# Kernel tuning notes

Hardware: AMD Instinct MI355X
Metric: run time of the kernel (lower is better)

The kernel has to match this reference:

```python
import jax, jax.numpy as jnp
import numpy as np

N_NODES = 100000
N_EDGES = 3200000


def gcn_conv(x, src, dst, ew, W, b, num_nodes):
    """PyG GCNConv: h = x@W; out[dst] += norm * h[src]; norm = d^-1/2[src]*w*d^-1/2[dst].
    src/dst/ew must already include self-loops (weight 1)."""
    h = x @ W  # [N, F_out]
    deg = jax.ops.segment_sum(ew, dst, num_segments=num_nodes)  # weighted in-degree
    dinv = jnp.where(deg > 0, jax.lax.rsqrt(deg), 0.0)
    norm = dinv[src] * ew * dinv[dst]  # [E]
    msg = h[src] * norm[:, None]  # [E, F_out] gather + scale
    out = jax.ops.segment_sum(msg, dst, num_segments=num_nodes)  # scatter-add
    return out + b


def setup_inputs() -> dict:
    key = jax.random.key(0)
    k1, k2, k3, k4, k5 = jax.random.split(key, 5)
    x = jax.random.normal(k1, (N_NODES, 35), dtype=jnp.float32)
    edge_index = jax.random.randint(k2, (2, N_EDGES), 0, N_NODES, dtype=jnp.int64)
    edge_weight = jax.random.uniform(k3, (N_EDGES,), dtype=jnp.float32)
    W1 = jax.random.normal(k4, (35, 64), dtype=jnp.float32) * (1.0 / np.sqrt(35))
    b1 = jnp.zeros((64,), dtype=jnp.float32)
    W2 = jax.random.normal(k5, (64, 2), dtype=jnp.float32) * (1.0 / np.sqrt(64))
    b2 = jnp.zeros((2,), dtype=jnp.float32)
    return {"x": x, "edge_index": edge_index, "edge_weight": edge_weight,
            "W1": W1, "b1": b1, "W2": W2, "b2": b2}


def reference(x, edge_index, edge_weight, W1, b1, W2, b2):
    n = x.shape[0]
    # add self-loops with weight 1 (PyG default fill_value=1), static shapes
    loop = jnp.arange(n, dtype=edge_index.dtype)
    src = jnp.concatenate([edge_index[0], loop])
    dst = jnp.concatenate([edge_index[1], loop])
    ew = jnp.concatenate([edge_weight, jnp.ones((n,), dtype=edge_weight.dtype)])

    h = jax.nn.relu(gcn_conv(x, src, dst, ew, W1, b1, n))
    h = gcn_conv(h, src, dst, ew, W2, b2, n)
    return jax.nn.log_softmax(h, axis=1)
```

## Files before the change

### kernel.cpp

```cpp
#include <hip/hip_runtime.h>
#include <hip/hip_fp16.h>
#include <math.h>

#define FIN 35
#define F1  64
#define BSZ 256
#define BSH 8
#define GSH 7
#define MAXNB 512
#define PCH 8192
#define SCAP 12288

__global__ void k_hist(const int* __restrict__ dst, int* __restrict__ cmat,
                       int E, int NB, int NCHUNK) {
    __shared__ int h[MAXNB];
    int c = blockIdx.x, t = threadIdx.x;
    for (int i = t; i < NB; i += 256) h[i] = 0;
    __syncthreads();
    int e0 = c * PCH, e1 = min(e0 + PCH, E);
    bool al = ((size_t)(dst + e0) & 15) == 0;
    int nv = al ? ((e1 - e0) >> 2) : 0;
    const int4* d4 = (const int4*)(dst + e0);
    for (int i = t; i < nv; i += 256) {
        int4 v = d4[i];
        atomicAdd(&h[v.x >> BSH], 1); atomicAdd(&h[v.y >> BSH], 1);
        atomicAdd(&h[v.z >> BSH], 1); atomicAdd(&h[v.w >> BSH], 1);
    }
    for (int e = e0 + (nv << 2) + t; e < e1; e += 256) atomicAdd(&h[dst[e] >> BSH], 1);
    __syncthreads();
    for (int i = t; i < NB; i += 256) cmat[(size_t)i * NCHUNK + c] = h[i];
}

__global__ void k_scan_row(int* __restrict__ cmat, int* __restrict__ rsum, int NCHUNK) {
    __shared__ int s[512];
    int b = blockIdx.x, t = threadIdx.x;
    int v = (t < NCHUNK) ? cmat[(size_t)b * NCHUNK + t] : 0;
    s[t] = v;
    __syncthreads();
    #pragma unroll
    for (int off = 1; off < 512; off <<= 1) {
        int tv = (t >= off) ? s[t - off] : 0;
        __syncthreads();
        s[t] += tv;
        __syncthreads();
    }
    if (t < NCHUNK) cmat[(size_t)b * NCHUNK + t] = s[t] - v;
    if (t == 511) rsum[b] = s[511];
}

__global__ void k_scan_buck(const int* __restrict__ rsum, int* __restrict__ bbase,
                            int* __restrict__ boff, int NB, int E) {
    __shared__ int s[1024];
    int t = threadIdx.x;
    int v = (t < NB) ? rsum[t] : 0;
    s[t] = v;
    __syncthreads();
    #pragma unroll
    for (int off = 1; off < 1024; off <<= 1) {
        int tv = (t >= off) ? s[t - off] : 0;
        __syncthreads();
        s[t] += tv;
        __syncthreads();
    }
    if (t < NB) {
        int excl = s[t] - v;
        bbase[t] = excl;
        boff[t] = excl;
    }
    if (t == 0) boff[NB] = E;
}

__global__ __launch_bounds__(512) void k_place(
        const int* __restrict__ src, const int* __restrict__ dst,
        const float* __restrict__ ew, const int* __restrict__ cmat,
        const int* __restrict__ bbase,
        int2* __restrict__ recs, int E, int NB, int NCHUNK) {
    extern __shared__ char pmem[];
    int2* lrec   = (int2*)pmem;
    int*  addr32 = (int*)(lrec + PCH);
    __shared__ int s[512];
    __shared__ int lbase[512];
    __shared__ int cur[512];
    __shared__ int gwin[512];
    int c = blockIdx.x, t = threadIdx.x;
    s[t] = 0;
    __syncthreads();
    int e0 = c * PCH, e1 = min(e0 + PCH, E);
    bool al = (((size_t)(dst + e0) | (size_t)(src + e0) | (size_t)(ew + e0)) & 15) == 0;
    int nv = al ? ((e1 - e0) >> 2) : 0;
    const int4*   s4 = (const int4*)(src + e0);
    const int4*   d4 = (const int4*)(dst + e0);
    const float4* w4 = (const float4*)(ew + e0);
    for (int i = t; i < nv; i += 512) {
        int4 v = d4[i];
        atomicAdd(&s[v.x >> BSH], 1); atomicAdd(&s[v.y >> BSH], 1);
        atomicAdd(&s[v.z >> BSH], 1); atomicAdd(&s[v.w >> BSH], 1);
    }
    for (int e = e0 + (nv << 2) + t; e < e1; e += 512) atomicAdd(&s[dst[e] >> BSH], 1);
    __syncthreads();
    int v = s[t];
    __syncthreads();
    #pragma unroll
    for (int off = 1; off < 512; off <<= 1) {
        int tv = (t >= off) ? s[t - off] : 0;
        __syncthreads();
        s[t] += tv;
        __syncthreads();
    }
    lbase[t] = s[t] - v;
    cur[t] = 0;
    gwin[t] = (t < NB) ? (cmat[(size_t)t * NCHUNK + c] + bbase[t]) : 0;
    __syncthreads();
    for (int i = t; i < nv; i += 512) {
        int4   sv = s4[i];
        int4   dv = d4[i];
        float4 wv = w4[i];
        int b, r, sl;
        b = dv.x >> BSH; r = atomicAdd(&cur[b], 1); sl = lbase[b] + r;
        lrec[sl] = make_int2(sv.x | ((dv.x & (BSZ-1)) << 24), __float_as_int(wv.x));
        addr32[sl] = gwin[b] + r;
        b = dv.y >> BSH; r = atomicAdd(&cur[b], 1); sl = lbase[b] + r;
        lrec[sl] = make_int2(sv.y | ((dv.y & (BSZ-1)) << 24), __float_as_int(wv.y));
        addr32[sl] = gwin[b] + r;
        b = dv.z >> BSH; r = atomicAdd(&cur[b], 1); sl = lbase[b] + r;
        lrec[sl] = make_int2(sv.z | ((dv.z & (BSZ-1)) << 24), __float_as_int(wv.z));
        addr32[sl] = gwin[b] + r;
        b = dv.w >> BSH; r = atomicAdd(&cur[b], 1); sl = lbase[b] + r;
        lrec[sl] = make_int2(sv.w | ((dv.w & (BSZ-1)) << 24), __float_as_int(wv.w));
        addr32[sl] = gwin[b] + r;
    }
    for (int e = e0 + (nv << 2) + t; e < e1; e += 512) {
        int d = dst[e];
        int b = d >> BSH;
        int r = atomicAdd(&cur[b], 1);
        int sl = lbase[b] + r;
        lrec[sl] = make_int2(src[e] | ((d & (BSZ-1)) << 24), __float_as_int(ew[e]));
        addr32[sl] = gwin[b] + r;
    }
    __syncthreads();
    int cnt = e1 - e0;
    for (int i = t; i < cnt; i += 512) recs[addr32[i]] = lrec[i];
}

__global__ __launch_bounds__(512) void k_sort(
        const int* __restrict__ boff, const int2* __restrict__ recs_in,
        int2* __restrict__ recs_out, int* __restrict__ row_ptr,
        float* __restrict__ dinv, int n) {
    extern __shared__ unsigned short inv16[];
    __shared__ int   hcnt[BSZ];
    __shared__ int   hoff[BSZ];
    __shared__ float dsum[BSZ];
    int b = blockIdx.x, t = threadIdx.x;
    if (t < BSZ) { hcnt[t] = 0; dsum[t] = 1.0f; }
    __syncthreads();
    int s0 = boff[b], s1 = boff[b + 1];
    int cnt = s1 - s0;
    for (int i = t; i < cnt; i += 512) {
        int2 rc = recs_in[s0 + i];
        int dl = ((unsigned)rc.x) >> 24;
        atomicAdd(&hcnt[dl], 1);
        atomicAdd(&dsum[dl], __int_as_float(rc.y));
    }
    __syncthreads();
    int v = 0;
    if (t < BSZ) { v = hcnt[t]; hoff[t] = v; }
    __syncthreads();
    #pragma unroll
    for (int off = 1; off < BSZ; off <<= 1) {
        int tv = 0;
        if (t < BSZ && t >= off) tv = hoff[t - off];
        __syncthreads();
        if (t < BSZ) hoff[t] += tv;
        __syncthreads();
    }
    if (t < BSZ) {
        int excl = hoff[t] - v;
        int node = b * BSZ + t;
        if (node < n) {
            row_ptr[node] = s0 + excl;
            dinv[node] = rsqrtf(dsum[t]);
            if (node == n - 1) row_ptr[n] = s1;
        }
        hcnt[t] = excl;
    }
    __syncthreads();
    if (cnt <= SCAP) {
        for (int i = t; i < cnt; i += 512) {
            int2 rc = recs_in[s0 + i];
            int dl = ((unsigned)rc.x) >> 24;
            int pos = atomicAdd(&hcnt[dl], 1);
            inv16[pos] = (unsigned short)i;
        }
        __syncthreads();
        for (int o = t; o < cnt; o += 512) {
            int2 rc = recs_in[s0 + inv16[o]];
            recs_out[s0 + o] = make_int2((rc.x & 0xFFFFFF) << GSH, rc.y);
        }
    } else {
        for (int i = t; i < cnt; i += 512) {
            int2 rc = recs_in[s0 + i];
            int dl = ((unsigned)rc.x) >> 24;
            int pos = atomicAdd(&hcnt[dl], 1);
            recs_out[s0 + pos] = make_int2((rc.x & 0xFFFFFF) << GSH, rc.y);
        }
    }
}

__global__ void k_gemm1(const float* __restrict__ x, const float* __restrict__ W1,
                        const float* __restrict__ dinv, __half* __restrict__ g1, int n) {
    __shared__ float W1s[FIN * F1];
    __shared__ float xs[64 * FIN];
    int t = threadIdx.x;
    for (int i = t; i < (FIN * F1) / 4; i += 256) ((float4*)W1s)[i] = ((const float4*)W1)[i];
    int row0 = blockIdx.x * 64;
    int nrows = min(64, n - row0);
    const float* xbase = x + (size_t)row0 * FIN;
    int tot = nrows * FIN;
    int totv = tot >> 2;
    for (int i = t; i < totv; i += 256) ((float4*)xs)[i] = ((const float4*)xbase)[i];
    for (int i = (totv << 2) + t; i < tot; i += 256) xs[i] = xbase[i];
    __syncthreads();
    int wave = t >> 6, f = t & 63;
    for (int rl = wave; rl < nrows; rl += 4) {
        float acc = 0.0f;
        #pragma unroll
        for (int k = 0; k < FIN; k++) acc += xs[rl * FIN + k] * W1s[k * F1 + f];
        int row = row0 + rl;
        g1[(size_t)row * F1 + f] = __float2half(acc * dinv[row]);
    }
}

__global__ void k_gather1(const int* __restrict__ rp, const int2* __restrict__ csr,
                          const __half* __restrict__ g1,
                          const float* __restrict__ dinv, const float* __restrict__ b1,
                          const float* __restrict__ W2, float* __restrict__ g2, int n) {
    int wid = (int)((blockIdx.x * (long long)blockDim.x + threadIdx.x) >> 6);
    int f = threadIdx.x & 63;
    if (wid >= n) return;
    const char* g1b = (const char*)g1 + f * 2;
    int start = rp[wid], end = rp[wid + 1];
    float acc = 0.0f;
    int e = start;
    for (; e + 16 <= end; e += 16) {
        float a[16];
        int2 r[16];
        #pragma unroll
        for (int j = 0; j < 16; j++) r[j] = csr[e + j];
        #pragma unroll
        for (int j = 0; j < 16; j++)
            a[j] = __half2float(*(const __half*)(g1b + (unsigned)r[j].x));
        #pragma unroll
        for (int j = 0; j < 16; j++) acc += __int_as_float(r[j].y) * a[j];
    }
    for (; e + 4 <= end; e += 4) {
        int2 r0 = csr[e], r1 = csr[e+1], r2 = csr[e+2], r3 = csr[e+3];
        float a0 = __half2float(*(const __half*)(g1b + (unsigned)r0.x));
        float a1 = __half2float(*(const __half*)(g1b + (unsigned)r1.x));
        float a2 = __half2float(*(const __half*)(g1b + (unsigned)r2.x));
        float a3 = __half2float(*(const __half*)(g1b + (unsigned)r3.x));
        acc += __int_as_float(r0.y) * a0; acc += __int_as_float(r1.y) * a1;
        acc += __int_as_float(r2.y) * a2; acc += __int_as_float(r3.y) * a3;
    }
    for (; e < end; e++) {
        int2 r = csr[e];
        acc += __int_as_float(r.y) * __half2float(*(const __half*)(g1b + (unsigned)r.x));
    }
    float dv = dinv[wid];
    float h = dv * (acc + __half2float(g1[(size_t)wid * F1 + f])) + b1[f];
    h = h > 0.0f ? h : 0.0f;
    float2 w2v = ((const float2*)W2)[f];
    float z0 = h * w2v.x, z1 = h * w2v.y;
    #pragma unroll
    for (int off = 32; off > 0; off >>= 1) {
        z0 += __shfl_xor(z0, off, 64);
        z1 += __shfl_xor(z1, off, 64);
    }
    if (f == 0) {
        g2[(size_t)wid * 2 + 0] = dv * z0;
        g2[(size_t)wid * 2 + 1] = dv * z1;
    }
}

__global__ void k_gather2(const int* __restrict__ rp, const int2* __restrict__ csr,
                          const float* __restrict__ g2,
                          const float* __restrict__ dinv, const float* __restrict__ b2,
                          float* __restrict__ out, int n) {
    int w = (int)((blockIdx.x * (long long)blockDim.x + threadIdx.x) >> 6);
    int lane = threadIdx.x & 63;
    int half = lane >> 5, sub = lane & 31;
    int node = w * 2 + half;
    if (node >= n) return;
    const char* g2b = (const char*)g2;
    int start = rp[node], end = rp[node + 1];
    float a0 = 0.0f, a1 = 0.0f;
    int e = start + sub;
    for (; e + 96 < end; e += 128) {
        int2 q0 = csr[e], q1 = csr[e + 32], q2 = csr[e + 64], q3 = csr[e + 96];
        float2 v0 = *(const float2*)(g2b + (((unsigned)q0.x) >> 4));
        float2 v1 = *(const float2*)(g2b + (((unsigned)q1.x) >> 4));
        float2 v2 = *(const float2*)(g2b + (((unsigned)q2.x) >> 4));
        float2 v3 = *(const float2*)(g2b + (((unsigned)q3.x) >> 4));
        a0 += __int_as_float(q0.y) * v0.x; a1 += __int_as_float(q0.y) * v0.y;
        a0 += __int_as_float(q1.y) * v1.x; a1 += __int_as_float(q1.y) * v1.y;
        a0 += __int_as_float(q2.y) * v2.x; a1 += __int_as_float(q2.y) * v2.y;
        a0 += __int_as_float(q3.y) * v3.x; a1 += __int_as_float(q3.y) * v3.y;
    }
    for (; e < end; e += 32) {
        int2 r = csr[e];
        float wt = __int_as_float(r.y);
        float2 gv = *(const float2*)(g2b + (((unsigned)r.x) >> 4));
        a0 += wt * gv.x; a1 += wt * gv.y;
    }
    #pragma unroll
    for (int off = 16; off > 0; off >>= 1) {
        a0 += __shfl_xor(a0, off, 64);
        a1 += __shfl_xor(a1, off, 64);
    }
    if (sub == 0) {
        float dv = dinv[node];
        float2 sv = ((const float2*)g2)[node];
        float z0 = dv * (a0 + sv.x) + b2[0];
        float z1 = dv * (a1 + sv.y) + b2[1];
        float m = fmaxf(z0, z1);
        float lse = m + logf(expf(z0 - m) + expf(z1 - m));
        ((float2*)out)[node] = make_float2(z0 - lse, z1 - lse);
    }
}

extern "C" void kernel_launch(void* const* d_in, const int* in_sizes, int n_in,
                              void* d_out, int out_size, void* d_ws, size_t ws_size,
                              hipStream_t stream) {
    const float* x  = (const float*)d_in[0];
    const int*   ei = (const int*)d_in[1];
    const float* ew = (const float*)d_in[2];
    const float* W1 = (const float*)d_in[3];
    const float* b1 = (const float*)d_in[4];
    const float* W2 = (const float*)d_in[5];
    const float* b2 = (const float*)d_in[6];
    float* out = (float*)d_out;

    int n = in_sizes[0] / FIN;
    int E = in_sizes[2];
    const int* src = ei;
    const int* dst = ei + E;
    int NB = (n + BSZ - 1) / BSZ;
    int NCHUNK = (E + PCH - 1) / PCH;
    int M = NB * NCHUNK;

    char* ws = (char*)d_ws;
    size_t off = 0;
    auto alloc = [&](size_t bytes) -> void* {
        void* p = ws + off;
        off += (bytes + 15) & ~(size_t)15;
        return p;
    };
    int*    cmat    = (int*)   alloc((size_t)M * 4);
    int*    rsum    = (int*)   alloc((size_t)NB * 4);
    int*    bbase   = (int*)   alloc((size_t)NB * 4);
    int*    boff    = (int*)   alloc((size_t)(NB + 1) * 4);
    int*    row_ptr = (int*)   alloc((size_t)(n + 1) * 4);
    float*  dinv    = (float*) alloc((size_t)n * 4);
    int2*   recs_a  = (int2*)  alloc((size_t)E * 8);
    int2*   recs_b  = (int2*)  alloc((size_t)E * 8);
    __half* g1      = (__half*)alloc((size_t)n * F1 * 2);
    float*  g2      = (float*) alloc((size_t)n * 2 * 4);

    size_t place_lds = (size_t)PCH * 8 + (size_t)PCH * 4;
    size_t sort_lds  = (size_t)SCAP * 2;

    int g2_waves = (n + 1) / 2 + 1;

    k_hist     <<<NCHUNK, 256, 0, stream>>>(dst, cmat, E, NB, NCHUNK);
    k_scan_row <<<NB, 512, 0, stream>>>(cmat, rsum, NCHUNK);
    k_scan_buck<<<1, 1024, 0, stream>>>(rsum, bbase, boff, NB, E);
    k_place    <<<NCHUNK, 512, place_lds, stream>>>(src, dst, ew, cmat, bbase, recs_a, E, NB, NCHUNK);
    k_sort     <<<NB, 512, sort_lds, stream>>>(boff, recs_a, recs_b, row_ptr, dinv, n);
    k_gemm1    <<<(n + 63) / 64, 256, 0, stream>>>(x, W1, dinv, g1, n);
    k_gather1  <<<(n + 3) / 4, 256, 0, stream>>>(row_ptr, recs_b, g1, dinv, b1, W2, g2, n);
    k_gather2  <<<(g2_waves + 3) / 4, 256, 0, stream>>>(row_ptr, recs_b, g2, dinv, b2, out, n);
}
```

Baseline: 299.8 us.

## Fuse layer-1 GEMM into bucket sort and coalesce placement writes per bucket

k_place no longer stores a per-record destination address. It copies each bucket's contiguous LDS run to its global window with half-waves, giving coalesced writes and less LDS. The x@W1 GEMM is folded into the tail of k_sort, reusing the block's in-LDS degree sums for the dinv scale, which removes one kernel launch and the dinv reread. The cost is more LDS per sort block, which may lower occupancy, and many small buckets may leave half-waves underused.

```diff
diff --git a/kernel.cpp b/kernel.cpp
--- a/kernel.cpp
+++ b/kernel.cpp
@@ -76,8 +76,7 @@
         const int* __restrict__ bbase,
         int2* __restrict__ recs, int E, int NB, int NCHUNK) {
     extern __shared__ char pmem[];
-    int2* lrec   = (int2*)pmem;
-    int*  addr32 = (int*)(lrec + PCH);
+    int2* lrec = (int2*)pmem;
     __shared__ int s[512];
     __shared__ int lbase[512];
     __shared__ int cur[512];
@@ -115,38 +114,39 @@
         int4   sv = s4[i];
         int4   dv = d4[i];
         float4 wv = w4[i];
-        int b, r, sl;
-        b = dv.x >> BSH; r = atomicAdd(&cur[b], 1); sl = lbase[b] + r;
-        lrec[sl] = make_int2(sv.x | ((dv.x & (BSZ-1)) << 24), __float_as_int(wv.x));
-        addr32[sl] = gwin[b] + r;
-        b = dv.y >> BSH; r = atomicAdd(&cur[b], 1); sl = lbase[b] + r;
-        lrec[sl] = make_int2(sv.y | ((dv.y & (BSZ-1)) << 24), __float_as_int(wv.y));
-        addr32[sl] = gwin[b] + r;
-        b = dv.z >> BSH; r = atomicAdd(&cur[b], 1); sl = lbase[b] + r;
-        lrec[sl] = make_int2(sv.z | ((dv.z & (BSZ-1)) << 24), __float_as_int(wv.z));
-        addr32[sl] = gwin[b] + r;
-        b = dv.w >> BSH; r = atomicAdd(&cur[b], 1); sl = lbase[b] + r;
-        lrec[sl] = make_int2(sv.w | ((dv.w & (BSZ-1)) << 24), __float_as_int(wv.w));
-        addr32[sl] = gwin[b] + r;
+        int b, r;
+        b = dv.x >> BSH; r = atomicAdd(&cur[b], 1);
+        lrec[lbase[b] + r] = make_int2(sv.x | ((dv.x & (BSZ-1)) << 24), __float_as_int(wv.x));
+        b = dv.y >> BSH; r = atomicAdd(&cur[b], 1);
+        lrec[lbase[b] + r] = make_int2(sv.y | ((dv.y & (BSZ-1)) << 24), __float_as_int(wv.y));
+        b = dv.z >> BSH; r = atomicAdd(&cur[b], 1);
+        lrec[lbase[b] + r] = make_int2(sv.z | ((dv.z & (BSZ-1)) << 24), __float_as_int(wv.z));
+        b = dv.w >> BSH; r = atomicAdd(&cur[b], 1);
+        lrec[lbase[b] + r] = make_int2(sv.w | ((dv.w & (BSZ-1)) << 24), __float_as_int(wv.w));
     }
     for (int e = e0 + (nv << 2) + t; e < e1; e += 512) {
         int d = dst[e];
         int b = d >> BSH;
         int r = atomicAdd(&cur[b], 1);
-        int sl = lbase[b] + r;
-        lrec[sl] = make_int2(src[e] | ((d & (BSZ-1)) << 24), __float_as_int(ew[e]));
-        addr32[sl] = gwin[b] + r;
-    }
-    __syncthreads();
-    int cnt = e1 - e0;
-    for (int i = t; i < cnt; i += 512) recs[addr32[i]] = lrec[i];
+        lrec[lbase[b] + r] = make_int2(src[e] | ((d & (BSZ-1)) << 24), __float_as_int(ew[e]));
+    }
+    __syncthreads();
+    int hw = t >> 5, sl = t & 31;
+    for (int b = hw; b < NB; b += 16) {
+        int lb = lbase[b], cn = cur[b], gw = gwin[b];
+        for (int i = sl; i < cn; i += 32) recs[gw + i] = lrec[lb + i];
+    }
 }
 
 __global__ __launch_bounds__(512) void k_sort(
         const int* __restrict__ boff, const int2* __restrict__ recs_in,
         int2* __restrict__ recs_out, int* __restrict__ row_ptr,
-        float* __restrict__ dinv, int n) {
-    extern __shared__ unsigned short inv16[];
+        float* __restrict__ dinv, const float* __restrict__ x,
+        const float* __restrict__ W1, __half* __restrict__ g1, int n) {
+    extern __shared__ char smem[];
+    unsigned short* inv16 = (unsigned short*)smem;
+    float* xs  = (float*)smem;
+    float* W1s = (float*)(smem + (size_t)BSZ * FIN * 4);
     __shared__ int   hcnt[BSZ];
     __shared__ int   hoff[BSZ];
     __shared__ float dsum[BSZ];
@@ -204,29 +204,23 @@
             recs_out[s0 + pos] = make_int2((rc.x & 0xFFFFFF) << GSH, rc.y);
         }
     }
-}
-
-__global__ void k_gemm1(const float* __restrict__ x, const float* __restrict__ W1,
-                        const float* __restrict__ dinv, __half* __restrict__ g1, int n) {
-    __shared__ float W1s[FIN * F1];
-    __shared__ float xs[64 * FIN];
-    int t = threadIdx.x;
-    for (int i = t; i < (FIN * F1) / 4; i += 256) ((float4*)W1s)[i] = ((const float4*)W1)[i];
-    int row0 = blockIdx.x * 64;
-    int nrows = min(64, n - row0);
+    __syncthreads();
+    int row0 = b * BSZ;
+    int nrows = min(BSZ, n - row0);
+    if (nrows <= 0) return;
+    for (int i = t; i < (FIN * F1) / 4; i += 512) ((float4*)W1s)[i] = ((const float4*)W1)[i];
     const float* xbase = x + (size_t)row0 * FIN;
     int tot = nrows * FIN;
     int totv = tot >> 2;
-    for (int i = t; i < totv; i += 256) ((float4*)xs)[i] = ((const float4*)xbase)[i];
-    for (int i = (totv << 2) + t; i < tot; i += 256) xs[i] = xbase[i];
-    __syncthreads();
-    int wave = t >> 6, f = t & 63;
-    for (int rl = wave; rl < nrows; rl += 4) {
+    for (int i = t; i < totv; i += 512) ((float4*)xs)[i] = ((const float4*)xbase)[i];
+    for (int i = (totv << 2) + t; i < tot; i += 512) xs[i] = xbase[i];
+    __syncthreads();
+    int f = t & 63, w8 = t >> 6;
+    for (int nl = w8; nl < nrows; nl += 8) {
         float acc = 0.0f;
         #pragma unroll
-        for (int k = 0; k < FIN; k++) acc += xs[rl * FIN + k] * W1s[k * F1 + f];
-        int row = row0 + rl;
-        g1[(size_t)row * F1 + f] = __float2half(acc * dinv[row]);
+        for (int k = 0; k < FIN; k++) acc += xs[nl * FIN + k] * W1s[k * F1 + f];
+        g1[(size_t)(row0 + nl) * F1 + f] = __float2half(acc * rsqrtf(dsum[nl]));
     }
 }
 
@@ -365,8 +359,8 @@
     __half* g1      = (__half*)alloc((size_t)n * F1 * 2);
     float*  g2      = (float*) alloc((size_t)n * 2 * 4);
 
-    size_t place_lds = (size_t)PCH * 8 + (size_t)PCH * 4;
-    size_t sort_lds  = (size_t)SCAP * 2;
+    size_t place_lds = (size_t)PCH * 8;
+    size_t sort_lds  = (size_t)BSZ * FIN * 4 + (size_t)FIN * F1 * 4;
 
     int g2_waves = (n + 1) / 2 + 1;
 
@@ -374,8 +368,7 @@
     k_scan_row <<<NB, 512, 0, stream>>>(cmat, rsum, NCHUNK);
     k_scan_buck<<<1, 1024, 0, stream>>>(rsum, bbase, boff, NB, E);
     k_place    <<<NCHUNK, 512, place_lds, stream>>>(src, dst, ew, cmat, bbase, recs_a, E, NB, NCHUNK);
-    k_sort     <<<NB, 512, sort_lds, stream>>>(boff, recs_a, recs_b, row_ptr, dinv, n);
-    k_gemm1    <<<(n + 63) / 64, 256, 0, stream>>>(x, W1, dinv, g1, n);
+    k_sort     <<<NB, 512, sort_lds, stream>>>(boff, recs_a, recs_b, row_ptr, dinv, x, W1, g1, n);
     k_gather1  <<<(n + 3) / 4, 256, 0, stream>>>(row_ptr, recs_b, g1, dinv, b1, W2, g2, n);
     k_gather2  <<<(g2_waves + 3) / 4, 256, 0, stream>>>(row_ptr, recs_b, g2, dinv, b2, out, n);
 }
```

After: 291.7 us (median of 2 runs). -2.7%, faster.
